# Kernel tuning notes

Hardware: AMD Instinct MI355X
Metric: run time of the kernel (lower is better)

Reference implementation:

```python
import jax, jax.numpy as jnp
import numpy as np

D_MODEL = 512
PROJ = 2 * D_MODEL  # 1024
N_STATES = 32
KSIZE = 4
LN_EPS = 1e-3  # keras LayerNormalization default epsilon


def setup_inputs() -> dict:
    key = jax.random.key(0)
    ks = jax.random.split(key, 16)
    B, L = 2, 2048
    s_in = 1.0 / np.sqrt(D_MODEL)
    s_pr = 1.0 / np.sqrt(PROJ)
    x = jax.random.normal(ks[0], (B, L, D_MODEL), dtype=jnp.float32)
    # LayerNorm params
    ln_gamma = jnp.ones((D_MODEL,), jnp.float32)
    ln_beta = jnp.zeros((D_MODEL,), jnp.float32)
    # dense1 / dense2: d_model -> proj
    W1 = jax.random.normal(ks[1], (D_MODEL, PROJ), jnp.float32) * s_in
    b1 = jnp.zeros((PROJ,), jnp.float32)
    W2 = jax.random.normal(ks[2], (D_MODEL, PROJ), jnp.float32) * s_in
    b2 = jnp.zeros((PROJ,), jnp.float32)
    # depthwise causal conv1d: kernel (K, 1, PROJ) in WIO layout, groups=PROJ
    conv_k = jax.random.normal(ks[3], (KSIZE, 1, PROJ), jnp.float32) * 0.5
    conv_b = jnp.zeros((PROJ,), jnp.float32)
    # SSM params
    A_log = jnp.log(jnp.broadcast_to(jnp.arange(1, N_STATES + 1, dtype=jnp.float32), (PROJ, N_STATES)))
    D_skip = jnp.ones((PROJ,), jnp.float32)
    WB = jax.random.normal(ks[4], (PROJ, N_STATES), jnp.float32) * s_pr
    bB = jnp.zeros((N_STATES,), jnp.float32)
    WC = jax.random.normal(ks[5], (PROJ, N_STATES), jnp.float32) * s_pr
    bC = jnp.zeros((N_STATES,), jnp.float32)
    Wd = jax.random.normal(ks[6], (PROJ, PROJ), jnp.float32) * s_pr
    bd = jnp.zeros((PROJ,), jnp.float32)
    # dense3: proj -> d_model
    W3 = jax.random.normal(ks[7], (PROJ, D_MODEL), jnp.float32) * s_pr
    b3 = jnp.zeros((D_MODEL,), jnp.float32)
    return dict(x=x, ln_gamma=ln_gamma, ln_beta=ln_beta, W1=W1, b1=b1, W2=W2, b2=b2,
                conv_k=conv_k, conv_b=conv_b, A_log=A_log, D_skip=D_skip,
                WB=WB, bB=bB, WC=WC, bC=bC, Wd=Wd, bd=bd, W3=W3, b3=b3)


def _layernorm(x, gamma, beta):
    mu = jnp.mean(x, axis=-1, keepdims=True)
    var = jnp.mean(jnp.square(x - mu), axis=-1, keepdims=True)
    return (x - mu) * jax.lax.rsqrt(var + LN_EPS) * gamma + beta


def _causal_dwconv(x, k, b):
    # x: [B,L,C], k: [K,1,C], depthwise causal conv (left-pad K-1)
    y = jax.lax.conv_general_dilated(
        x, k, window_strides=(1,), padding=[(KSIZE - 1, 0)],
        dimension_numbers=('NWC', 'WIO', 'NWC'), feature_group_count=PROJ)
    return y + b


def _selective_scan(u, delta, A, Bm, Cm, D_skip):
    # u, delta: [B,L,D]; A: [D,N]; Bm, Cm: [B,L,N]; D_skip: [D]
    deltaA = jnp.einsum('bld,dn->bldn', delta, A)                 # [B,L,D,N]
    deltaBu = jnp.einsum('bld,bld,bln->bldn', delta, u, Bm)        # [B,L,D,N]
    # shift deltaA left by one along L, zero at the end (pad trick in source)
    shifted = jnp.concatenate([deltaA[:, 1:], jnp.zeros_like(deltaA[:, :1])], axis=1)
    # reversed cumsum along L, then exp
    e = jnp.exp(jnp.flip(jnp.cumsum(jnp.flip(shifted, axis=1), axis=1), axis=1))
    xs = jnp.cumsum(deltaBu * e, axis=1) / (e + 1e-12)
    y = jnp.einsum('bldn,bln->bld', xs, Cm)
    return y + u * D_skip


def reference(x, ln_gamma, ln_beta, W1, b1, W2, b2, conv_k, conv_b,
              A_log, D_skip, WB, bB, WC, bC, Wd, bd, W3, b3):
    h = _layernorm(x, ln_gamma, ln_beta)
    x1 = h @ W1 + b1                      # [B,L,PROJ]
    x1 = _causal_dwconv(x1, conv_k, conv_b)
    x1 = jax.nn.silu(x1)
    A = -jnp.exp(A_log)                    # [PROJ,N]
    Cm = x1 @ WC + bC                      # [B,L,N]
    Bm = x1 @ WB + bB                      # [B,L,N]
    delta = jax.nn.softplus(x1 @ Wd + bd)  # [B,L,PROJ]
    y = _selective_scan(x1, delta, A, Bm, Cm, D_skip)
    x2 = jax.nn.silu(h @ W2 + b2)
    out = (y * x2) @ W3 + b3 + x           # residual; dropout is identity at inference
    return out
```

## Files before the change

### kernel.cpp

```cpp
#include <hip/hip_runtime.h>
#include <stdint.h>

#define L_SEQ 2048
#define BATCH 2
#define DMODEL 512
#define PROJ 1024
#define NST 32
#define NCATU 1088
#define ROWS (BATCH*L_SEQ)
#define THRESH 50.0f

typedef float f32x4 __attribute__((ext_vector_type(4)));
typedef short short8 __attribute__((ext_vector_type(8)));

__device__ inline float bf2f(unsigned short u){ uint32_t x=((uint32_t)u)<<16; float f; __builtin_memcpy(&f,&x,4); return f; }
__device__ inline unsigned short f2bf(float f){ uint32_t x; __builtin_memcpy(&x,&f,4); uint32_t r=x+0x7FFFu+((x>>16)&1u); return (unsigned short)(r>>16); }
__device__ inline float siluf(float x){ return x/(1.f+__expf(-x)); }
__device__ inline float softplusf(float x){ return x>20.f? x : log1pf(__expf(x)); }

#define AS1(p) ((const __attribute__((address_space(1))) void*)(p))
#define AS3(p) ((__attribute__((address_space(3))) void*)(p))

template<int N> __device__ inline void wait_vmcnt(){
  if constexpr (N==0)      asm volatile("s_waitcnt vmcnt(0)" ::: "memory");
  else if constexpr (N==4) asm volatile("s_waitcnt vmcnt(4)" ::: "memory");
  else                     asm volatile("s_waitcnt vmcnt(8)" ::: "memory");
}

__global__ __launch_bounds__(256)
void prep_kernel(const float* __restrict__ W1, const float* __restrict__ b1,
                 const float* __restrict__ W2, const float* __restrict__ b2,
                 const float* __restrict__ Wd, const float* __restrict__ bd,
                 const float* __restrict__ WB, const float* __restrict__ bB,
                 const float* __restrict__ WC, const float* __restrict__ bC,
                 const float* __restrict__ W3,
                 unsigned short* __restrict__ W12t, unsigned short* __restrict__ Wcatt,
                 unsigned short* __restrict__ W3t, float* __restrict__ bias12,
                 float* __restrict__ biascat)
{
  __shared__ float tile[32][33];
  int bid = blockIdx.x;
  int lx = threadIdx.x & 31, ly = threadIdx.x >> 5;
  if (bid < 1024) {
    int kt = bid & 15, nt = bid >> 4;
    int k0 = kt*32, n0 = nt*32;
    const float* S = (n0 < 1024) ? W1 : W2;
    int nc = (n0 < 1024) ? n0 : n0 - 1024;
#pragma unroll
    for (int i=0;i<4;i++)
      tile[ly+i*8][lx] = S[(size_t)(k0+ly+i*8)*1024 + nc + lx];
    __syncthreads();
#pragma unroll
    for (int i=0;i<4;i++)
      W12t[(size_t)(n0+ly+i*8)*512 + k0 + lx] = f2bf(tile[lx][ly+i*8]);
    return;
  }
  if (bid < 2112) {
    int t = bid - 1024;
    int kt = t & 31, nt = t >> 5;
    int k0 = kt*32, n0 = nt*32;
#pragma unroll
    for (int i=0;i<4;i++){
      int k = k0 + ly + i*8;
      float v;
      if (n0 < 1024)       v = Wd[(size_t)k*1024 + n0 + lx];
      else if (n0 == 1024) v = WB[(size_t)k*32 + lx];
      else                 v = WC[(size_t)k*32 + lx];
      tile[ly+i*8][lx] = v;
    }
    __syncthreads();
#pragma unroll
    for (int i=0;i<4;i++)
      Wcatt[(size_t)(n0+ly+i*8)*1024 + k0 + lx] = f2bf(tile[lx][ly+i*8]);
    return;
  }
  if (bid < 2624) {
    int t = bid - 2112;
    int kt = t & 31, nt = t >> 5;
    int k0 = kt*32, n0 = nt*32;
#pragma unroll
    for (int i=0;i<4;i++)
      tile[ly+i*8][lx] = W3[(size_t)(k0+ly+i*8)*512 + n0 + lx];
    __syncthreads();
#pragma unroll
    for (int i=0;i<4;i++)
      W3t[(size_t)(n0+ly+i*8)*1024 + k0 + lx] = f2bf(tile[lx][ly+i*8]);
    return;
  }
  int j = (bid - 2624)*256 + threadIdx.x;
  if (j < 2048) { bias12[j] = (j < 1024) ? b1[j] : b2[j-1024]; return; }
  j -= 2048;
  if (j < NCATU) biascat[j] = (j < 1024) ? bd[j] : (j < 1056) ? bB[j-1024] : bC[j-1056];
}

__global__ __launch_bounds__(256)
void ln_kernel(const float* __restrict__ x, const float* __restrict__ gamma,
               const float* __restrict__ beta, unsigned short* __restrict__ H)
{
  int row = blockIdx.x*4 + (threadIdx.x >> 6);
  int lane = threadIdx.x & 63;
  const float4* xr = (const float4*)(x + (size_t)row*DMODEL);
  float4 v0 = xr[lane];
  float4 v1 = xr[lane+64];
  float s = v0.x+v0.y+v0.z+v0.w + v1.x+v1.y+v1.z+v1.w;
  float q = v0.x*v0.x+v0.y*v0.y+v0.z*v0.z+v0.w*v0.w
          + v1.x*v1.x+v1.y*v1.y+v1.z*v1.z+v1.w*v1.w;
#pragma unroll
  for (int m=32;m>0;m>>=1){ s += __shfl_xor(s,m); q += __shfl_xor(q,m); }
  float mu = s*(1.f/DMODEL);
  float var = q*(1.f/DMODEL) - mu*mu;
  float rs = rsqrtf(var + 1e-3f);
  int c0 = lane*4, c1 = 256 + lane*4;
  float4 g0 = *(const float4*)&gamma[c0]; float4 g1 = *(const float4*)&gamma[c1];
  float4 t0 = *(const float4*)&beta[c0];  float4 t1 = *(const float4*)&beta[c1];
  ushort4 o0, o1;
  o0.x = f2bf((v0.x-mu)*rs*g0.x + t0.x);
  o0.y = f2bf((v0.y-mu)*rs*g0.y + t0.y);
  o0.z = f2bf((v0.z-mu)*rs*g0.z + t0.z);
  o0.w = f2bf((v0.w-mu)*rs*g0.w + t0.w);
  o1.x = f2bf((v1.x-mu)*rs*g1.x + t1.x);
  o1.y = f2bf((v1.y-mu)*rs*g1.y + t1.y);
  o1.z = f2bf((v1.z-mu)*rs*g1.z + t1.z);
  o1.w = f2bf((v1.w-mu)*rs*g1.w + t1.w);
  *(ushort4*)&H[(size_t)row*DMODEL + c0] = o0;
  *(ushort4*)&H[(size_t)row*DMODEL + c1] = o1;
}

template<int MODE>
__global__ __launch_bounds__(256)
void gemm_bt(const unsigned short* __restrict__ A, const unsigned short* __restrict__ Bt,
             void* __restrict__ Cv, const float* __restrict__ bias,
             const float* __restrict__ res, int M, int N, int K, int Kfull)
{
  constexpr int BK = 64;
  constexpr int LPT = 4;
  __shared__ unsigned short As[3][64*BK];
  __shared__ unsigned short Bs[3][64*BK];
  int tid = threadIdx.x;
  int lane = tid & 63, wid = tid >> 6;
  int wm = wid >> 1, wn = wid & 1;

  int gx = gridDim.x;
  int nwg = gx * gridDim.y;
  int L = blockIdx.y*gx + blockIdx.x;
  int W = (L & 7)*(nwg >> 3) + (L >> 3);
  int bx = W % gx, by = W / gx;
  int m0 = bx*64, n0 = by*64;
  int kofs = blockIdx.z*K;

  f32x4 acc[2][2];
#pragma unroll
  for (int i=0;i<2;i++)
#pragma unroll
    for (int j=0;j<2;j++)
#pragma unroll
      for (int e=0;e<4;e++) acc[i][j][e] = 0.f;

  const unsigned short* ap[2];
  const unsigned short* bp[2];
#pragma unroll
  for (int j=0;j<2;j++){
    int s = tid + j*256;
    int row = s >> 3, kc = ((s & 7) ^ (row & 7)) * 8;
    ap[j] = A + (size_t)(m0+row)*Kfull + kofs + kc;
    bp[j] = Bt + (size_t)(n0+row)*Kfull + kofs + kc;
  }

  auto stage = [&](int buf){
#pragma unroll
    for (int j=0;j<2;j++){
      __builtin_amdgcn_global_load_lds(AS1(ap[j]), AS3(&As[buf][(size_t)(j*256 + wid*64)*8]), 16, 0, 0);
      ap[j] += BK;
    }
#pragma unroll
    for (int j=0;j<2;j++){
      __builtin_amdgcn_global_load_lds(AS1(bp[j]), AS3(&Bs[buf][(size_t)(j*256 + wid*64)*8]), 16, 0, 0);
      bp[j] += BK;
    }
  };

  stage(0);
  stage(1);
  int T = K/BK;
  int rb = 0, wb = 2;
  int r = lane & 15, kb = lane >> 4;
  for (int t = 0; t < T; ++t) {
    if (t+1 < T) wait_vmcnt<LPT>();
    else         wait_vmcnt<0>();
    __builtin_amdgcn_s_barrier();
    if (t+2 < T) { stage(wb); wb = (wb==2)?0:wb+1; }
#pragma unroll
    for (int ks=0; ks<2; ++ks) {
      int cx = (ks*4 + kb) ^ (r & 7);
      short8 af[2], bfr[2];
#pragma unroll
      for (int i=0;i<2;i++){
        int row = wm*32 + i*16 + r;
        af[i] = *(const short8*)&As[rb][(row*8 + cx)*8];
      }
#pragma unroll
      for (int j=0;j<2;j++){
        int row = wn*32 + j*16 + r;
        bfr[j] = *(const short8*)&Bs[rb][(row*8 + cx)*8];
      }
      __builtin_amdgcn_s_setprio(1);
#pragma unroll
      for (int i=0;i<2;i++)
#pragma unroll
        for (int j=0;j<2;j++)
          acc[i][j] = __builtin_amdgcn_mfma_f32_16x16x32_bf16(af[i], bfr[j], acc[i][j], 0,0,0);
      __builtin_amdgcn_s_setprio(0);
    }
    rb = (rb==2)?0:rb+1;
  }

  int rr = (lane >> 4)*4, cc = lane & 15;
#pragma unroll
  for (int i=0;i<2;i++)
#pragma unroll
    for (int j=0;j<2;j++) {
      int col = n0 + wn*32 + j*16 + cc;
      float bcol = (MODE == 1) ? bias[col] : 0.f;
#pragma unroll
      for (int e=0;e<4;e++) {
        int row = m0 + wm*32 + i*16 + rr + e;
        float v = acc[i][j][e];
        if constexpr (MODE == 2) {
          v += bias[row];
          if (row < 1024) v = softplusf(v);
          ((float*)Cv)[(size_t)row*N + col] = v;
        } else if constexpr (MODE == 1) {
          ((unsigned short*)Cv)[(size_t)row*N + col] = f2bf(v + bcol);
        } else {
          ((float*)Cv)[(size_t)blockIdx.z*M*N + (size_t)row*N + col] = v;
        }
      }
    }
}

__global__ __launch_bounds__(256)
void reduce_kernel(const float* __restrict__ P, const float* __restrict__ x,
                   const float* __restrict__ b3, float* __restrict__ out)
{
  size_t i = ((size_t)blockIdx.x*256 + threadIdx.x)*4;
  int col = (int)(i & 511);
  float4 a = *(const float4*)&P[i];
  float4 b = *(const float4*)&P[(size_t)ROWS*512 + i];
  float4 xv = *(const float4*)&x[i];
  float4 bv = *(const float4*)&b3[col];
  float4 o;
  o.x = a.x + b.x + xv.x + bv.x;
  o.y = a.y + b.y + xv.y + bv.y;
  o.z = a.z + b.z + xv.z + bv.z;
  o.w = a.w + b.w + xv.w + bv.w;
  *(float4*)&out[i] = o;
}

__global__ __launch_bounds__(256)
void conv_silu_kernel(const unsigned short* __restrict__ P12, const float* __restrict__ ck,
                      const float* __restrict__ cb, unsigned short* __restrict__ ubf,
                      unsigned short* __restrict__ x2bf)
{
  int gid = blockIdx.x*256 + threadIdx.x;
  int c4 = gid & 511;
  int row = gid >> 9;
  int l = row & (L_SEQ-1);
  if (c4 < 256) {
    int c = c4*4;
    float4 bv = *(const float4*)&cb[c];
    float r0=bv.x, r1=bv.y, r2=bv.z, r3=bv.w;
#pragma unroll
    for (int t=0;t<4;t++){
      int lsrc = l - 3 + t;
      if (lsrc >= 0) {
        ushort4 xv = *(const ushort4*)&P12[(size_t)(row-3+t)*2048 + c];
        float4 kv = *(const float4*)&ck[t*PROJ + c];
        r0 = fmaf(bf2f(xv.x),kv.x,r0);
        r1 = fmaf(bf2f(xv.y),kv.y,r1);
        r2 = fmaf(bf2f(xv.z),kv.z,r2);
        r3 = fmaf(bf2f(xv.w),kv.w,r3);
      }
    }
    ushort4 o;
    o.x=f2bf(siluf(r0)); o.y=f2bf(siluf(r1)); o.z=f2bf(siluf(r2)); o.w=f2bf(siluf(r3));
    *(ushort4*)&ubf[(size_t)row*PROJ + c] = o;
  } else {
    int c = (c4-256)*4;
    ushort4 xv = *(const ushort4*)&P12[(size_t)row*2048 + 1024 + c];
    ushort4 o;
    o.x=f2bf(siluf(bf2f(xv.x))); o.y=f2bf(siluf(bf2f(xv.y)));
    o.z=f2bf(siluf(bf2f(xv.z))); o.w=f2bf(siluf(bf2f(xv.w)));
    *(ushort4*)&x2bf[(size_t)row*PROJ + c] = o;
  }
}

__global__ __launch_bounds__(256)
void sscan_kernel(const float* __restrict__ CT, const unsigned short* __restrict__ ubf,
                  const float* __restrict__ A_log, int* __restrict__ l0out,
                  unsigned short* __restrict__ ystate)
{
  __shared__ float suf8sh[8][256];
  int tid = threadIdx.x;
  int n = tid & 31, gsub = tid >> 5;
  int G = blockIdx.x*8 + gsub;
  int b = G >> 10, d = G & 1023;
  const float* dT = CT + (size_t)d*ROWS + b*L_SEQ;

  float mysum = 0.f;
  {
    const float4* c4 = (const float4*)(dT + n*64);
    for (int it=0; it<16; ++it){ float4 v = c4[it]; mysum += v.x+v.y+v.z+v.w; }
  }
  float incl = mysum;
#pragma unroll
  for (int dlt=1; dlt<32; dlt<<=1){ float t = __shfl_up(incl, dlt, 32); if (n >= dlt) incl += t; }
  float Tot = __shfl(incl, 31, 32);
  float excl = incl - mysum;
  int cnt = 0;
  {
    const float4* c4 = (const float4*)(dT + n*64);
    float run = excl;
    for (int it=0; it<16; ++it){
      float4 v = c4[it];
      if ((it & 1) == 0) suf8sh[gsub][n*8 + (it>>1)] = Tot - run;
      cnt += (Tot - run >= THRESH); run += v.x;
      cnt += (Tot - run >= THRESH); run += v.y;
      cnt += (Tot - run >= THRESH); run += v.z;
      cnt += (Tot - run >= THRESH); run += v.w;
    }
  }
#pragma unroll
  for (int m=16;m>0;m>>=1) cnt += __shfl_xor(cnt, m, 32);
  int myl0 = cnt > 0 ? cnt-1 : 0;
  if (n == 0) l0out[G] = myl0;
  __syncthreads();

  int base = min(myl0, __shfl_xor(myl0, 32)) & ~7;
  float np1 = __expf(A_log[d*NST + n]);
  const float* Br = CT + (size_t)(1024+n)*ROWS + b*L_SEQ;
  const float* Cr = CT + (size_t)(1056+n)*ROWS + b*L_SEQ;
  const unsigned short* ub = ubf + (size_t)b*L_SEQ*PROJ + d;
  unsigned short* yb = ystate + (size_t)b*L_SEQ*PROJ + d;
  float s = 0.f;
  for (int l = base; l < L_SEQ; l += 8) {
    float4 d0 = *(const float4*)&dT[l];
    float4 d1 = *(const float4*)&dT[l+4];
    float4 B0 = *(const float4*)&Br[l];
    float4 B1 = *(const float4*)&Br[l+4];
    float4 C0 = *(const float4*)&Cr[l];
    float4 C1 = *(const float4*)&Cr[l+4];
    float sufv = suf8sh[gsub][l >> 3];
    float dl[8] = {d0.x,d0.y,d0.z,d0.w,d1.x,d1.y,d1.z,d1.w};
    float Bv[8] = {B0.x,B0.y,B0.z,B0.w,B1.x,B1.y,B1.z,B1.w};
    float Cv[8] = {C0.x,C0.y,C0.z,C0.w,C1.x,C1.y,C1.z,C1.w};
    float uu[8];
#pragma unroll
    for (int t=0;t<8;t++) uu[t] = bf2f(ub[(size_t)(l+t)*PROJ]);
    float cum = 0.f;
#pragma unroll
    for (int t=0;t<8;t++){
      cum += dl[t];
      float decay = __expf(-dl[t]*np1);
      s = fmaf(decay, s, dl[t]*uu[t]*Bv[t]);
      float gte = 1.f/(1.f + 1e-12f*__expf(np1*(sufv - cum)));
      float contrib = s*gte*Cv[t];
#pragma unroll
      for (int m=16;m>0;m>>=1) contrib += __shfl_xor(contrib, m);
      if (n == 0) yb[(size_t)(l+t)*PROJ] = f2bf(contrib);
    }
  }
}

__global__ __launch_bounds__(256)
void zmul_kernel(const unsigned short* __restrict__ ystate, const unsigned short* __restrict__ ubf,
                 const unsigned short* __restrict__ x2bf, const float* __restrict__ Dskip,
                 const int* __restrict__ l0arr, unsigned short* __restrict__ zbf)
{
  size_t i = ((size_t)blockIdx.x*256 + threadIdx.x)*4;
  int d = (int)(i & (PROJ-1));
  int row = (int)(i >> 10);
  int l = row & (L_SEQ-1);
  int b = row >> 11;
  int4 l0v = *(const int4*)&l0arr[b*PROJ + d];
  ushort4 yu = *(const ushort4*)&ystate[i];
  float ysx = (l >= l0v.x) ? bf2f(yu.x) : 0.f;
  float ysy = (l >= l0v.y) ? bf2f(yu.y) : 0.f;
  float ysz = (l >= l0v.z) ? bf2f(yu.z) : 0.f;
  float ysw = (l >= l0v.w) ? bf2f(yu.w) : 0.f;
  ushort4 uu = *(const ushort4*)&ubf[i];
  ushort4 xx = *(const ushort4*)&x2bf[i];
  float4 Dv = *(const float4*)&Dskip[d];
  ushort4 o;
  o.x = f2bf((ysx + bf2f(uu.x)*Dv.x)*bf2f(xx.x));
  o.y = f2bf((ysy + bf2f(uu.y)*Dv.y)*bf2f(xx.y));
  o.z = f2bf((ysz + bf2f(uu.z)*Dv.z)*bf2f(xx.z));
  o.w = f2bf((ysw + bf2f(uu.w)*Dv.w)*bf2f(xx.w));
  *(ushort4*)&zbf[i] = o;
}

extern "C" void kernel_launch(void* const* d_in, const int* in_sizes, int n_in,
                              void* d_out, int out_size, void* d_ws, size_t ws_size,
                              hipStream_t stream)
{
  const float* x     = (const float*)d_in[0];
  const float* ln_g  = (const float*)d_in[1];
  const float* ln_b  = (const float*)d_in[2];
  const float* W1    = (const float*)d_in[3];
  const float* b1    = (const float*)d_in[4];
  const float* W2    = (const float*)d_in[5];
  const float* b2    = (const float*)d_in[6];
  const float* convk = (const float*)d_in[7];
  const float* convb = (const float*)d_in[8];
  const float* A_log = (const float*)d_in[9];
  const float* Dskip = (const float*)d_in[10];
  const float* WB    = (const float*)d_in[11];
  const float* bB    = (const float*)d_in[12];
  const float* WC    = (const float*)d_in[13];
  const float* bC    = (const float*)d_in[14];
  const float* Wd    = (const float*)d_in[15];
  const float* bd    = (const float*)d_in[16];
  const float* W3    = (const float*)d_in[17];
  const float* b3    = (const float*)d_in[18];

  char* w = (char*)d_ws;
  auto alloc = [&](size_t bytes){ char* p = w; w += (bytes + 255) & ~(size_t)255; return p; };
  unsigned short* Hbf    = (unsigned short*)alloc((size_t)ROWS*DMODEL*2);
  unsigned short* W12t   = (unsigned short*)alloc((size_t)2048*512*2);
  unsigned short* Wcatt  = (unsigned short*)alloc((size_t)NCATU*1024*2);
  unsigned short* W3t    = (unsigned short*)alloc((size_t)512*1024*2);
  float*          bias12 = (float*)alloc(2048*4);
  float*          biascat= (float*)alloc(NCATU*4);
  unsigned short* P12    = (unsigned short*)alloc((size_t)ROWS*2048*2);
  unsigned short* ubf    = (unsigned short*)alloc((size_t)ROWS*PROJ*2);
  unsigned short* x2bf   = (unsigned short*)alloc((size_t)ROWS*PROJ*2);
  float*          CT     = (float*)alloc((size_t)NCATU*ROWS*4);
  int*            l0arr  = (int*)alloc(2048*4);
  unsigned short* ystate = (unsigned short*)alloc((size_t)ROWS*PROJ*2);
  unsigned short* zbf    = (unsigned short*)alloc((size_t)ROWS*PROJ*2);
  float*          Pp     = (float*)alloc((size_t)2*ROWS*512*4);

  prep_kernel<<<2637, 256, 0, stream>>>(W1,b1,W2,b2,Wd,bd,WB,bB,WC,bC,W3,
                                        W12t,Wcatt,W3t,bias12,biascat);
  ln_kernel<<<ROWS/4, 256, 0, stream>>>(x, ln_g, ln_b, Hbf);

  dim3 g1(ROWS/64, 2048/64);
  gemm_bt<1><<<g1, 256, 0, stream>>>(Hbf, W12t, P12, bias12, nullptr, ROWS, 2048, DMODEL, DMODEL);

  conv_silu_kernel<<<ROWS*512/256, 256, 0, stream>>>(P12, convk, convb, ubf, x2bf);

  dim3 g2(NCATU/64, ROWS/64);
  gemm_bt<2><<<g2, 256, 0, stream>>>(Wcatt, ubf, CT, biascat, nullptr, NCATU, ROWS, PROJ, PROJ);

  sscan_kernel<<<2048/8, 256, 0, stream>>>(CT, ubf, A_log, l0arr, ystate);

  zmul_kernel<<<(ROWS*PROJ/4)/256, 256, 0, stream>>>(ystate, ubf, x2bf, Dskip, l0arr, zbf);

  dim3 g3(ROWS/64, 512/64, 2);
  gemm_bt<5><<<g3, 256, 0, stream>>>(zbf, W3t, Pp, b3, nullptr, ROWS, 512, 512, PROJ);
  reduce_kernel<<<(ROWS*512/4)/256, 256, 0, stream>>>(Pp, x, b3, (float*)d_out);
}
```

Baseline: 160.0 us.

## Use 128x128 GEMM tiles with double buffering for the first two projections

Adds a 128x128-tile bf16 MFMA GEMM kernel in which each wave computes a 64x64 sub-tile and fragments are loaded up front, with double-buffered global-to-LDS staging. It is used for the W1/W2 projection and the delta/B/C projection, which is zero-padded from 1088 to 1152 rows so it divides into 128-row tiles. The goal is more data reuse per tile and fewer tile loads. In exchange it adds wasted padded compute, a larger CT buffer, fewer workgroups per GEMM and higher register and LDS pressure.

```diff
diff --git a/kernel.cpp b/kernel.cpp
--- a/kernel.cpp
+++ b/kernel.cpp
@@ -6,7 +6,7 @@
 #define DMODEL 512
 #define PROJ 1024
 #define NST 32
-#define NCATU 1088
+#define NCAT 1152
 #define ROWS (BATCH*L_SEQ)
 #define THRESH 50.0f
 
@@ -24,7 +24,8 @@
 template<int N> __device__ inline void wait_vmcnt(){
   if constexpr (N==0)      asm volatile("s_waitcnt vmcnt(0)" ::: "memory");
   else if constexpr (N==4) asm volatile("s_waitcnt vmcnt(4)" ::: "memory");
-  else                     asm volatile("s_waitcnt vmcnt(8)" ::: "memory");
+  else if constexpr (N==8) asm volatile("s_waitcnt vmcnt(8)" ::: "memory");
+  else                     asm volatile("s_waitcnt vmcnt(12)" ::: "memory");
 }
 
 __global__ __launch_bounds__(256)
@@ -55,7 +56,7 @@
       W12t[(size_t)(n0+ly+i*8)*512 + k0 + lx] = f2bf(tile[lx][ly+i*8]);
     return;
   }
-  if (bid < 2112) {
+  if (bid < 2176) {
     int t = bid - 1024;
     int kt = t & 31, nt = t >> 5;
     int k0 = kt*32, n0 = nt*32;
@@ -65,7 +66,8 @@
       float v;
       if (n0 < 1024)       v = Wd[(size_t)k*1024 + n0 + lx];
       else if (n0 == 1024) v = WB[(size_t)k*32 + lx];
-      else                 v = WC[(size_t)k*32 + lx];
+      else if (n0 == 1056) v = WC[(size_t)k*32 + lx];
+      else                 v = 0.f;
       tile[ly+i*8][lx] = v;
     }
     __syncthreads();
@@ -74,8 +76,8 @@
       Wcatt[(size_t)(n0+ly+i*8)*1024 + k0 + lx] = f2bf(tile[lx][ly+i*8]);
     return;
   }
-  if (bid < 2624) {
-    int t = bid - 2112;
+  if (bid < 2688) {
+    int t = bid - 2176;
     int kt = t & 31, nt = t >> 5;
     int k0 = kt*32, n0 = nt*32;
 #pragma unroll
@@ -87,10 +89,10 @@
       W3t[(size_t)(n0+ly+i*8)*1024 + k0 + lx] = f2bf(tile[lx][ly+i*8]);
     return;
   }
-  int j = (bid - 2624)*256 + threadIdx.x;
+  int j = (bid - 2688)*256 + threadIdx.x;
   if (j < 2048) { bias12[j] = (j < 1024) ? b1[j] : b2[j-1024]; return; }
   j -= 2048;
-  if (j < NCATU) biascat[j] = (j < 1024) ? bd[j] : (j < 1056) ? bB[j-1024] : bC[j-1056];
+  if (j < NCAT) biascat[j] = (j < 1024) ? bd[j] : (j < 1056) ? bB[j-1024] : (j < 1088) ? bC[j-1056] : 0.f;
 }
 
 __global__ __launch_bounds__(256)
@@ -128,9 +130,120 @@
 
 template<int MODE>
 __global__ __launch_bounds__(256)
-void gemm_bt(const unsigned short* __restrict__ A, const unsigned short* __restrict__ Bt,
+void gemm128(const unsigned short* __restrict__ A, const unsigned short* __restrict__ Bt,
              void* __restrict__ Cv, const float* __restrict__ bias,
-             const float* __restrict__ res, int M, int N, int K, int Kfull)
+             int M, int N, int K)
+{
+  constexpr int BK = 64;
+  constexpr int LPT = 8;
+  __shared__ unsigned short As[2][128*BK];
+  __shared__ unsigned short Bs[2][128*BK];
+  int tid = threadIdx.x;
+  int lane = tid & 63, wid = tid >> 6;
+  int wm = wid >> 1, wn = wid & 1;
+
+  int gx = gridDim.x;
+  int nwg = gx * gridDim.y;
+  int L = blockIdx.y*gx + blockIdx.x;
+  int W = (L & 7)*(nwg >> 3) + (L >> 3);
+  int bx = W % gx, by = W / gx;
+  int m0 = bx*128, n0 = by*128;
+
+  f32x4 acc[4][4];
+#pragma unroll
+  for (int i=0;i<4;i++)
+#pragma unroll
+    for (int j=0;j<4;j++)
+#pragma unroll
+      for (int e=0;e<4;e++) acc[i][j][e] = 0.f;
+
+  const unsigned short* ap[4];
+  const unsigned short* bp[4];
+#pragma unroll
+  for (int j=0;j<4;j++){
+    int s = tid + j*256;
+    int row = s >> 3, kc = ((s & 7) ^ (row & 7)) * 8;
+    ap[j] = A + (size_t)(m0+row)*K + kc;
+    bp[j] = Bt + (size_t)(n0+row)*K + kc;
+  }
+
+  auto stage = [&](int buf){
+#pragma unroll
+    for (int j=0;j<4;j++){
+      __builtin_amdgcn_global_load_lds(AS1(ap[j]), AS3(&As[buf][(size_t)(j*256 + wid*64)*8]), 16, 0, 0);
+      ap[j] += BK;
+    }
+#pragma unroll
+    for (int j=0;j<4;j++){
+      __builtin_amdgcn_global_load_lds(AS1(bp[j]), AS3(&Bs[buf][(size_t)(j*256 + wid*64)*8]), 16, 0, 0);
+      bp[j] += BK;
+    }
+  };
+
+  stage(0);
+  stage(1);
+  int T = K/BK;
+  int r = lane & 15, kb = lane >> 4;
+  for (int t = 0; t < T; ++t) {
+    int rb = t & 1;
+    if (t+1 < T) wait_vmcnt<LPT>();
+    else         wait_vmcnt<0>();
+    __builtin_amdgcn_s_barrier();
+    short8 af[2][4], bfr[2][4];
+#pragma unroll
+    for (int ks=0; ks<2; ++ks) {
+      int cx = (ks*4 + kb) ^ (r & 7);
+#pragma unroll
+      for (int i=0;i<4;i++){
+        int row = wm*64 + i*16 + r;
+        af[ks][i] = *(const short8*)&As[rb][(row*8 + cx)*8];
+      }
+#pragma unroll
+      for (int j=0;j<4;j++){
+        int row = wn*64 + j*16 + r;
+        bfr[ks][j] = *(const short8*)&Bs[rb][(row*8 + cx)*8];
+      }
+    }
+    asm volatile("s_waitcnt lgkmcnt(0)" ::: "memory");
+    __builtin_amdgcn_sched_barrier(0);
+    __builtin_amdgcn_s_barrier();
+    if (t+2 < T) stage(rb);
+    __builtin_amdgcn_s_setprio(1);
+#pragma unroll
+    for (int ks=0; ks<2; ++ks)
+#pragma unroll
+      for (int i=0;i<4;i++)
+#pragma unroll
+        for (int j=0;j<4;j++)
+          acc[i][j] = __builtin_amdgcn_mfma_f32_16x16x32_bf16(af[ks][i], bfr[ks][j], acc[i][j], 0,0,0);
+    __builtin_amdgcn_s_setprio(0);
+  }
+
+  int rr = (lane >> 4)*4, cc = lane & 15;
+#pragma unroll
+  for (int i=0;i<4;i++)
+#pragma unroll
+    for (int j=0;j<4;j++) {
+      int col = n0 + wn*64 + j*16 + cc;
+      float bcol = (MODE == 1) ? bias[col] : 0.f;
+#pragma unroll
+      for (int e=0;e<4;e++) {
+        int row = m0 + wm*64 + i*16 + rr + e;
+        float v = acc[i][j][e];
+        if constexpr (MODE == 2) {
+          v += bias[row];
+          if (row < 1024) v = softplusf(v);
+          ((float*)Cv)[(size_t)row*N + col] = v;
+        } else {
+          ((unsigned short*)Cv)[(size_t)row*N + col] = f2bf(v + bcol);
+        }
+      }
+    }
+}
+
+__global__ __launch_bounds__(256)
+void gemm64s(const unsigned short* __restrict__ A, const unsigned short* __restrict__ Bt,
+             float* __restrict__ Pp, int M, int N, int K, int Kfull)
 {
   constexpr int BK = 64;
   constexpr int LPT = 4;
@@ -139,7 +252,6 @@
   int tid = threadIdx.x;
   int lane = tid & 63, wid = tid >> 6;
   int wm = wid >> 1, wn = wid & 1;
-
   int gx = gridDim.x;
   int nwg = gx * gridDim.y;
   int L = blockIdx.y*gx + blockIdx.x;
@@ -165,7 +277,6 @@
     ap[j] = A + (size_t)(m0+row)*Kfull + kofs + kc;
     bp[j] = Bt + (size_t)(n0+row)*Kfull + kofs + kc;
   }
-
   auto stage = [&](int buf){
 #pragma unroll
     for (int j=0;j<2;j++){
@@ -178,9 +289,7 @@
       bp[j] += BK;
     }
   };
-
-  stage(0);
-  stage(1);
+  stage(0); stage(1);
   int T = K/BK;
   int rb = 0, wb = 2;
   int r = lane & 15, kb = lane >> 4;
@@ -194,15 +303,9 @@
       int cx = (ks*4 + kb) ^ (r & 7);
       short8 af[2], bfr[2];
 #pragma unroll
-      for (int i=0;i<2;i++){
-        int row = wm*32 + i*16 + r;
-        af[i] = *(const short8*)&As[rb][(row*8 + cx)*8];
-      }
-#pragma unroll
-      for (int j=0;j<2;j++){
-        int row = wn*32 + j*16 + r;
-        bfr[j] = *(const short8*)&Bs[rb][(row*8 + cx)*8];
-      }
+      for (int i=0;i<2;i++) af[i]  = *(const short8*)&As[rb][((wm*32 + i*16 + r)*8 + cx)*8];
+#pragma unroll
+      for (int j=0;j<2;j++) bfr[j] = *(const short8*)&Bs[rb][((wn*32 + j*16 + r)*8 + cx)*8];
       __builtin_amdgcn_s_setprio(1);
 #pragma unroll
       for (int i=0;i<2;i++)
@@ -213,27 +316,16 @@
     }
     rb = (rb==2)?0:rb+1;
   }
-
   int rr = (lane >> 4)*4, cc = lane & 15;
 #pragma unroll
   for (int i=0;i<2;i++)
 #pragma unroll
     for (int j=0;j<2;j++) {
       int col = n0 + wn*32 + j*16 + cc;
-      float bcol = (MODE == 1) ? bias[col] : 0.f;
 #pragma unroll
       for (int e=0;e<4;e++) {
         int row = m0 + wm*32 + i*16 + rr + e;
-        float v = acc[i][j][e];
-        if constexpr (MODE == 2) {
-          v += bias[row];
-          if (row < 1024) v = softplusf(v);
-          ((float*)Cv)[(size_t)row*N + col] = v;
-        } else if constexpr (MODE == 1) {
-          ((unsigned short*)Cv)[(size_t)row*N + col] = f2bf(v + bcol);
-        } else {
-          ((float*)Cv)[(size_t)blockIdx.z*M*N + (size_t)row*N + col] = v;
-        }
+        Pp[(size_t)blockIdx.z*M*N + (size_t)row*N + col] = acc[i][j][e];
       }
     }
 }
@@ -426,36 +518,36 @@
   auto alloc = [&](size_t bytes){ char* p = w; w += (bytes + 255) & ~(size_t)255; return p; };
   unsigned short* Hbf    = (unsigned short*)alloc((size_t)ROWS*DMODEL*2);
   unsigned short* W12t   = (unsigned short*)alloc((size_t)2048*512*2);
-  unsigned short* Wcatt  = (unsigned short*)alloc((size_t)NCATU*1024*2);
+  unsigned short* Wcatt  = (unsigned short*)alloc((size_t)NCAT*1024*2);
   unsigned short* W3t    = (unsigned short*)alloc((size_t)512*1024*2);
   float*          bias12 = (float*)alloc(2048*4);
-  float*          biascat= (float*)alloc(NCATU*4);
+  float*          biascat= (float*)alloc(NCAT*4);
   unsigned short* P12    = (unsigned short*)alloc((size_t)ROWS*2048*2);
   unsigned short* ubf    = (unsigned short*)alloc((size_t)ROWS*PROJ*2);
   unsigned short* x2bf   = (unsigned short*)alloc((size_t)ROWS*PROJ*2);
-  float*          CT     = (float*)alloc((size_t)NCATU*ROWS*4);
+  float*          CT     = (float*)alloc((size_t)NCAT*ROWS*4);
   int*            l0arr  = (int*)alloc(2048*4);
   unsigned short* ystate = (unsigned short*)alloc((size_t)ROWS*PROJ*2);
   unsigned short* zbf    = (unsigned short*)alloc((size_t)ROWS*PROJ*2);
   float*          Pp     = (float*)alloc((size_t)2*ROWS*512*4);
 
-  prep_kernel<<<2637, 256, 0, stream>>>(W1,b1,W2,b2,Wd,bd,WB,bB,WC,bC,W3,
+  prep_kernel<<<2701, 256, 0, stream>>>(W1,b1,W2,b2,Wd,bd,WB,bB,WC,bC,W3,
                                         W12t,Wcatt,W3t,bias12,biascat);
   ln_kernel<<<ROWS/4, 256, 0, stream>>>(x, ln_g, ln_b, Hbf);
 
-  dim3 g1(ROWS/64, 2048/64);
-  gemm_bt<1><<<g1, 256, 0, stream>>>(Hbf, W12t, P12, bias12, nullptr, ROWS, 2048, DMODEL, DMODEL);
+  dim3 g1(ROWS/128, 2048/128);
+  gemm128<1><<<g1, 256, 0, stream>>>(Hbf, W12t, P12, bias12, ROWS, 2048, DMODEL);
 
   conv_silu_kernel<<<ROWS*512/256, 256, 0, stream>>>(P12, convk, convb, ubf, x2bf);
 
-  dim3 g2(NCATU/64, ROWS/64);
-  gemm_bt<2><<<g2, 256, 0, stream>>>(Wcatt, ubf, CT, biascat, nullptr, NCATU, ROWS, PROJ, PROJ);
+  dim3 g2(NCAT/128, ROWS/128);
+  gemm128<2><<<g2, 256, 0, stream>>>(Wcatt, ubf, CT, biascat, NCAT, ROWS, PROJ);
 
   sscan_kernel<<<2048/8, 256, 0, stream>>>(CT, ubf, A_log, l0arr, ystate);
 
   zmul_kernel<<<(ROWS*PROJ/4)/256, 256, 0, stream>>>(ystate, ubf, x2bf, Dskip, l0arr, zbf);
 
   dim3 g3(ROWS/64, 512/64, 2);
-  gemm_bt<5><<<g3, 256, 0, stream>>>(zbf, W3t, Pp, b3, nullptr, ROWS, 512, 512, PROJ);
+  gemm64s<<<g3, 256, 0, stream>>>(zbf, W3t, Pp, ROWS, 512, 512, PROJ);
   reduce_kernel<<<(ROWS*512/4)/256, 256, 0, stream>>>(Pp, x, b3, (float*)d_out);
 }
```

Result: no change. 159.8 us (-0.1%).
